# Performance work log

Hardware: AMD Instinct MI355X
Metric: run time of the kernel (lower is better)

## Reference

```python
import jax, jax.numpy as jnp
import numpy as np

H = 12            # num_heads
GRID = 14         # sqrt(num_patches)
NP_ = GRID * GRID # num_patches = 196


def _relative_position_index():
    coords = np.stack(np.meshgrid(np.arange(GRID), np.arange(GRID), indexing='ij'))  # [2,14,14]
    flat = coords.reshape(2, -1)                                   # [2,196]
    rel = flat[:, :, None] - flat[:, None, :]                      # [2,196,196]
    rel = rel.transpose(1, 2, 0).astype(np.int32)                  # [196,196,2]
    rel[..., 0] += GRID - 1
    rel[..., 1] += GRID - 1
    rel[..., 0] *= 2 * GRID - 1
    return rel.sum(-1)                                             # [196,196] in [0,729)


def setup_inputs() -> dict:
    key = jax.random.key(0)
    k1, k2, k3, k4 = jax.random.split(key, 4)
    B, N, C = 64, NP_ + 1, 768
    return {
        'x': jax.random.normal(k1, (B, N, C), dtype=jnp.float32),
        'w_qkv': jax.random.normal(k2, (3 * C, C), dtype=jnp.float32) * 0.02,
        'w_proj': jax.random.normal(k3, (C, C), dtype=jnp.float32) * 0.02,
        'b_proj': jnp.zeros((C,), dtype=jnp.float32),
        # torch inits the table to zeros; use small randn so the bias path is exercised
        'rpb_table': jax.random.normal(k4, ((2 * GRID - 1) ** 2, H), dtype=jnp.float32) * 0.02,
        'rel_idx': jnp.asarray(_relative_position_index()),
    }


def reference(x, w_qkv, w_proj, b_proj, rpb_table, rel_idx):
    B, N, C = x.shape
    hd = C // H
    scale = hd ** -0.5
    qkv = (x @ w_qkv.T).reshape(B, N, 3, H, hd).transpose(2, 0, 3, 1, 4)  # [3,B,H,N,hd]
    q, k, v = qkv[0] * scale, qkv[1], qkv[2]
    attn = jnp.einsum('bhqd,bhkd->bhqk', q, k)                            # [B,H,N,N]
    bias = rpb_table[rel_idx.reshape(-1)].reshape(NP_, NP_, H).transpose(2, 0, 1)  # [H,196,196]
    attn = attn.at[:, :, 1:, 1:].add(bias[None])                          # skip CLS row/col
    attn = jax.nn.softmax(attn, axis=-1)
    out = jnp.einsum('bhqk,bhkd->bqhd', attn, v).reshape(B, N, C)
    return out @ w_proj.T + b_proj
```

## Files before the change

### kernel.cpp

```cpp
#include <hip/hip_runtime.h>

typedef float f32x4 __attribute__((ext_vector_type(4)));
typedef short short8 __attribute__((ext_vector_type(8)));

#define DEVI static __device__ __forceinline__

DEVI ushort f2bf(float f) {
  unsigned u = __builtin_bit_cast(unsigned, f);
  u += 0x7fffu + ((u >> 16) & 1u);
  return (ushort)(u >> 16);
}

DEVI float b2f(ushort u) {
  unsigned x = ((unsigned)u) << 16;
  return __builtin_bit_cast(float, x);
}

DEVI short8 pack8(float4 a, float4 b) {
  union { ushort u[8]; short8 v; } t;
  t.u[0] = f2bf(a.x); t.u[1] = f2bf(a.y); t.u[2] = f2bf(a.z); t.u[3] = f2bf(a.w);
  t.u[4] = f2bf(b.x); t.u[5] = f2bf(b.y); t.u[6] = f2bf(b.z); t.u[7] = f2bf(b.w);
  return t.v;
}

DEVI f32x4 MFMA16(short8 a, short8 b, f32x4 c) {
  return __builtin_amdgcn_mfma_f32_16x16x32_bf16(a, b, c, 0, 0, 0);
}

DEVI void gld16(const ushort* g, ushort* l) {
  __builtin_amdgcn_global_load_lds(
      (const __attribute__((address_space(1))) unsigned int*)g,
      (__attribute__((address_space(3))) unsigned int*)l, 16, 0, 0);
}

#define VMC0() asm volatile("s_waitcnt vmcnt(0)" ::: "memory")
#define LGK0() asm volatile("s_waitcnt lgkmcnt(0)" ::: "memory")

__global__ void prep_all(const float* __restrict__ table, const int* __restrict__ rel_idx,
                         ushort* __restrict__ bias,
                         const float* __restrict__ x, ushort* __restrict__ xbf,
                         const float* __restrict__ wq, ushort* __restrict__ wqb,
                         const float* __restrict__ wp, ushort* __restrict__ wpb) {
  const int bid = blockIdx.x, tid = threadIdx.x;
  if (bid < 2028) {
    int i = bid * 256 + tid;
    int k = i % 208;
    int t = i / 208;
    int q = t % 208;
    int h = t / 208;
    float v;
    if (k >= 197) v = -1e30f;
    else if (q == 0 || k == 0 || q >= 197) v = 0.0f;
    else v = table[rel_idx[(q - 1) * 196 + (k - 1)] * 12 + h];
    bias[i] = f2bf(v);
  } else if (bid < 6756) {
    int i = (bid - 2028) * 256 + tid;
    float4 a = ((const float4*)x)[i * 2];
    float4 b = ((const float4*)x)[i * 2 + 1];
    ((short8*)xbf)[i] = pack8(a, b);
  } else if (bid < 7620) {
    int i = (bid - 6756) * 256 + tid;
    float4 a = ((const float4*)wq)[i * 2];
    float4 b = ((const float4*)wq)[i * 2 + 1];
    ((short8*)wqb)[i] = pack8(a, b);
  } else {
    int i = (bid - 7620) * 256 + tid;
    float4 a = ((const float4*)wp)[i * 2];
    float4 b = ((const float4*)wp)[i * 2 + 1];
    ((short8*)wpb)[i] = pack8(a, b);
  }
}

template <int MODE, int NBN>
__launch_bounds__(256, 4)
__global__ void gemm128(const ushort* __restrict__ A, const ushort* __restrict__ B,
                        ushort* __restrict__ q, ushort* __restrict__ k,
                        ushort* __restrict__ v,
                        const float* __restrict__ bprj, float* __restrict__ out) {
  __shared__ __align__(16) ushort As[2][4096];
  __shared__ __align__(16) ushort Bs[2][4096];

  const int tid = threadIdx.x;
  const int lane = tid & 63, wid = tid >> 6;
  const int wm = wid >> 1, wn = wid & 1;
  const int l15 = lane & 15, l4 = lane >> 4;

  const int nwg = gridDim.x;
  const int qc = nwg >> 3, rc = nwg & 7;
  const int xcd = blockIdx.x & 7, sub = blockIdx.x >> 3;
  const int wgid = (xcd < rc ? xcd * (qc + 1) : rc * (qc + 1) + (xcd - rc) * qc) + sub;
  const int bn = wgid % NBN, bm = wgid / NBN;

  const int c0 = wid * 2, c1 = wid * 2 + 1;
  const int r0 = c0 * 16 + (lane >> 2);
  const int r1 = c1 * 16 + (lane >> 2);
  const int g = lane & 3;
  const int col0 = (g << 3) ^ ((r0 & 6) << 2);
  const int col1 = (g << 3) ^ ((r1 & 6) << 2);
  long ar0 = bm * 128 + r0; if (ar0 > 12607) ar0 = 12607;
  long ar1 = bm * 128 + r1; if (ar1 > 12607) ar1 = 12607;
  const ushort* pA0 = A + ar0 * 768 + col0;
  const ushort* pA1 = A + ar1 * 768 + col1;
  const ushort* pB0 = B + (size_t)(bn * 128 + r0) * 768 + col0;
  const ushort* pB1 = B + (size_t)(bn * 128 + r1) * 768 + col1;

  const int xk = (l4 * 8) ^ ((l15 & 6) << 2);
  int aoff[4], boff[4];
#pragma unroll
  for (int m = 0; m < 4; m++) aoff[m] = (wm * 64 + m * 16 + l15) * 32 + xk;
#pragma unroll
  for (int n = 0; n < 4; n++) boff[n] = (wn * 64 + n * 16 + l15) * 32 + xk;

  f32x4 acc[4][4];
#pragma unroll
  for (int m = 0; m < 4; m++)
#pragma unroll
    for (int n = 0; n < 4; n++) acc[m][n] = (f32x4)0.0f;

#define STAGE(BUF, KO)                          \
  gld16(pA0 + (KO), &As[BUF][c0 * 512]);        \
  gld16(pA1 + (KO), &As[BUF][c1 * 512]);        \
  gld16(pB0 + (KO), &Bs[BUF][c0 * 512]);        \
  gld16(pB1 + (KO), &Bs[BUF][c1 * 512]);

#define COMPUTE(BUF)                                                \
  {                                                                 \
    short8 af[4], bv[4];                                            \
    _Pragma("unroll") for (int m = 0; m < 4; m++)                   \
        af[m] = *(const short8*)&As[BUF][aoff[m]];                  \
    _Pragma("unroll") for (int n = 0; n < 4; n++)                   \
        bv[n] = *(const short8*)&Bs[BUF][boff[n]];                  \
    __builtin_amdgcn_s_setprio(1);                                  \
    _Pragma("unroll") for (int m = 0; m < 4; m++)                   \
        _Pragma("unroll") for (int n = 0; n < 4; n++)               \
            acc[m][n] = MFMA16(af[m], bv[n], acc[m][n]);            \
    __builtin_amdgcn_s_setprio(0);                                  \
  }

  STAGE(0, 0)
  for (int t = 0; t < 23; ++t) {
    VMC0(); LGK0();
    __builtin_amdgcn_s_barrier();
    __builtin_amdgcn_sched_barrier(0);
    STAGE((t + 1) & 1, (t + 1) * 32)
    COMPUTE(t & 1)
  }
  VMC0(); LGK0();
  __builtin_amdgcn_s_barrier();
  __builtin_amdgcn_sched_barrier(0);
  COMPUTE(1)

  if (MODE == 0) {
    const int s = bn / 6;
    ushort* dst = (s == 0) ? q : ((s == 1) ? k : v);
    const float qs = (s == 0) ? 0.125f : 1.0f;
    const int cbase = bn * 128 + wn * 64 - s * 768;
    const int hh = cbase >> 6;
#pragma unroll
    for (int m = 0; m < 4; m++) {
#pragma unroll
      for (int r = 0; r < 4; r++) {
        int gm = bm * 128 + wm * 64 + m * 16 + l4 * 4 + r;
        if (gm >= 12608) continue;
        int b = gm / 197;
        int ns = gm - b * 197;
        size_t base = (size_t)((b * 12 + hh) * 197 + ns) * 64;
#pragma unroll
        for (int n = 0; n < 4; n++)
          dst[base + n * 16 + l15] = f2bf(acc[m][n][r] * qs);
      }
    }
  } else {
    float bb[4];
#pragma unroll
    for (int n = 0; n < 4; n++) bb[n] = bprj[bn * 128 + wn * 64 + n * 16 + l15];
#pragma unroll
    for (int m = 0; m < 4; m++) {
#pragma unroll
      for (int r = 0; r < 4; r++) {
        int gm = bm * 128 + wm * 64 + m * 16 + l4 * 4 + r;
        if (gm >= 12608) continue;
#pragma unroll
        for (int n = 0; n < 4; n++)
          out[(size_t)gm * 768 + bn * 128 + wn * 64 + n * 16 + l15] = acc[m][n][r] + bb[n];
      }
    }
  }
#undef STAGE
#undef COMPUTE
}

__launch_bounds__(832)
__global__ void attn(const ushort* __restrict__ qws, const ushort* __restrict__ kws,
                     const ushort* __restrict__ vws, const ushort* __restrict__ biasws,
                     ushort* __restrict__ aout) {
  __shared__ __align__(16) ushort Ks[208 * 72];
  __shared__ __align__(16) ushort Vt[64 * 232];
  __shared__ __align__(16) ushort Ps[13 * 16 * 232];

  const int bh = blockIdx.x;
  const int b = bh / 12;
  const int h = bh - b * 12;
  const ushort* qb = qws + (size_t)bh * 197 * 64;
  const ushort* kb = kws + (size_t)bh * 197 * 64;
  const ushort* vb = vws + (size_t)bh * 197 * 64;

  const int tid = threadIdx.x;
  const int lane = tid & 63, wid = tid >> 6;
  const int l15 = lane & 15, l4 = lane >> 4;

  for (int c = tid; c < 208 * 8; c += 832) {
    int n = c >> 3, col = (c & 7) << 3;
    short8 v = (short8)0;
    if (n < 197) v = *(const short8*)(kb + n * 64 + col);
    *(short8*)&Ks[n * 72 + col] = v;
  }
  for (int c = tid; c < 224 * 8; c += 832) {
    int n = c % 224;
    int d0 = (c / 224) << 3;
    ushort tmp[8] = {0, 0, 0, 0, 0, 0, 0, 0};
    if (n < 197) {
      short8 v = *(const short8*)(vb + n * 64 + d0);
#pragma unroll
      for (int j = 0; j < 8; j++) tmp[j] = (ushort)v[j];
    }
#pragma unroll
    for (int j = 0; j < 8; j++) Vt[(d0 + j) * 232 + n] = tmp[j];
  }
  __syncthreads();

  ushort* pb = &Ps[wid * (16 * 232)];
  const ushort* biasb = biasws + (size_t)h * 208 * 208;

  {
    const int t = wid;
    const int q0 = t * 16;
    int qr = q0 + l15; if (qr > 196) qr = 196;
    short8 aq0 = *(const short8*)(qb + qr * 64 + (l4 << 3));
    short8 aq1 = *(const short8*)(qb + qr * 64 + 32 + (l4 << 3));

    f32x4 sc[13];
    __builtin_amdgcn_s_setprio(1);
#pragma unroll
    for (int ct = 0; ct < 13; ct++) {
      short8 b0 = *(const short8*)&Ks[(ct * 16 + l15) * 72 + (l4 << 3)];
      short8 b1 = *(const short8*)&Ks[(ct * 16 + l15) * 72 + 32 + (l4 << 3)];
      f32x4 s = (f32x4)0.0f;
      s = MFMA16(aq0, b0, s);
      s = MFMA16(aq1, b1, s);
      sc[ct] = s;
    }
    __builtin_amdgcn_s_setprio(0);

    float mx[4] = {-1e38f, -1e38f, -1e38f, -1e38f};
#pragma unroll
    for (int ct = 0; ct < 13; ct++) {
#pragma unroll
      for (int r = 0; r < 4; r++) {
        float bv = b2f(biasb[(q0 + l4 * 4 + r) * 208 + ct * 16 + l15]);
        float v = sc[ct][r] + bv;
        sc[ct][r] = v;
        mx[r] = fmaxf(mx[r], v);
      }
    }
#pragma unroll
    for (int r = 0; r < 4; r++) {
      mx[r] = fmaxf(mx[r], __shfl_xor(mx[r], 1));
      mx[r] = fmaxf(mx[r], __shfl_xor(mx[r], 2));
      mx[r] = fmaxf(mx[r], __shfl_xor(mx[r], 4));
      mx[r] = fmaxf(mx[r], __shfl_xor(mx[r], 8));
    }
    float sum[4] = {0.f, 0.f, 0.f, 0.f};
#pragma unroll
    for (int ct = 0; ct < 13; ct++) {
#pragma unroll
      for (int r = 0; r < 4; r++) {
        float p = __expf(sc[ct][r] - mx[r]);
        sc[ct][r] = p;
        sum[r] += p;
      }
    }
#pragma unroll
    for (int r = 0; r < 4; r++) {
      sum[r] += __shfl_xor(sum[r], 1);
      sum[r] += __shfl_xor(sum[r], 2);
      sum[r] += __shfl_xor(sum[r], 4);
      sum[r] += __shfl_xor(sum[r], 8);
    }

#pragma unroll
    for (int ct = 0; ct < 13; ct++)
#pragma unroll
      for (int r = 0; r < 4; r++)
        pb[(l4 * 4 + r) * 232 + ct * 16 + l15] = f2bf(sc[ct][r]);
#pragma unroll
    for (int r = 0; r < 4; r++)
      pb[(l4 * 4 + r) * 232 + 208 + l15] = 0;

    short8 pa[7];
#pragma unroll
    for (int kk = 0; kk < 7; kk++)
      pa[kk] = *(const short8*)&pb[l15 * 232 + kk * 32 + (l4 << 3)];
    f32x4 o[4];
    __builtin_amdgcn_s_setprio(1);
#pragma unroll
    for (int dt = 0; dt < 4; dt++) {
      f32x4 acc = (f32x4)0.0f;
#pragma unroll
      for (int kk = 0; kk < 7; kk++) {
        short8 bv = *(const short8*)&Vt[(dt * 16 + l15) * 232 + kk * 32 + (l4 << 3)];
        acc = MFMA16(pa[kk], bv, acc);
      }
      o[dt] = acc;
    }
    __builtin_amdgcn_s_setprio(0);

    float rs[4];
#pragma unroll
    for (int r = 0; r < 4; r++) rs[r] = 1.0f / sum[r];
#pragma unroll
    for (int dt = 0; dt < 4; dt++) {
#pragma unroll
      for (int r = 0; r < 4; r++) {
        int row = q0 + l4 * 4 + r;
        if (row < 197) {
          float v = o[dt][r] * rs[r];
          aout[(size_t)(b * 197 + row) * 768 + h * 64 + dt * 16 + l15] = f2bf(v);
        }
      }
    }
  }
}

extern "C" void kernel_launch(void* const* d_in, const int* in_sizes, int n_in,
                              void* d_out, int out_size, void* d_ws, size_t ws_size,
                              hipStream_t stream) {
  const float* x      = (const float*)d_in[0];
  const float* w_qkv  = (const float*)d_in[1];
  const float* w_proj = (const float*)d_in[2];
  const float* b_proj = (const float*)d_in[3];
  const float* rpb    = (const float*)d_in[4];
  const int*   relidx = (const int*)d_in[5];
  float* out = (float*)d_out;

  char* ws = (char*)d_ws;
  const size_t HB = (size_t)12608 * 768 * 2;
  ushort* xbf   = (ushort*)(ws);
  ushort* qws   = (ushort*)(ws + HB);
  ushort* kws   = (ushort*)(ws + 2 * HB);
  ushort* vws   = (ushort*)(ws + 3 * HB);
  ushort* bias  = (ushort*)(ws + 4 * HB);
  ushort* wqkvb = (ushort*)(ws + 4 * HB + 2076672);
  ushort* wprjb = (ushort*)(ws + 4 * HB + 2076672 + 3538944);
  ushort* aout  = xbf;

  hipLaunchKernelGGL(prep_all, dim3(7908), dim3(256), 0, stream,
                     rpb, relidx, bias, x, xbf, w_qkv, wqkvb, w_proj, wprjb);
  hipLaunchKernelGGL((gemm128<0, 18>), dim3(18 * 99), dim3(256), 0, stream,
                     xbf, wqkvb, qws, kws, vws, nullptr, nullptr);
  hipLaunchKernelGGL(attn, dim3(768), dim3(832), 0, stream, qws, kws, vws, bias, aout);
  hipLaunchKernelGGL((gemm128<1, 6>), dim3(6 * 99), dim3(256), 0, stream,
                     aout, wprjb, nullptr, nullptr, nullptr, b_proj, out);
}
```

Baseline: 132.5 us.

## Process two query tiles per wave in attention to reuse K/V LDS fragments

Attention kernel now uses 7 waves of 448 threads instead of 13, each wave computing 32 query rows (two 16-row MFMA tiles) so every K and V fragment read from LDS feeds two MFMAs. The output stores are interleaved into the PV loop, and bias row indices are clamped for the padded rows. GEMM launch bounds are also raised to 5 waves per SIMD occupancy. This cuts LDS traffic per MFMA but raises register pressure (26 score accumulators per wave) and lowers the thread count per block. Higher GEMM occupancy may force spills.

```diff
diff --git a/kernel.cpp b/kernel.cpp
--- a/kernel.cpp
+++ b/kernel.cpp
@@ -72,7 +72,7 @@
 }
 
 template <int MODE, int NBN>
-__launch_bounds__(256, 4)
+__launch_bounds__(256, 5)
 __global__ void gemm128(const ushort* __restrict__ A, const ushort* __restrict__ B,
                         ushort* __restrict__ q, ushort* __restrict__ k,
                         ushort* __restrict__ v,
@@ -190,13 +190,13 @@
 #undef COMPUTE
 }
 
-__launch_bounds__(832)
+__launch_bounds__(448)
 __global__ void attn(const ushort* __restrict__ qws, const ushort* __restrict__ kws,
                      const ushort* __restrict__ vws, const ushort* __restrict__ biasws,
                      ushort* __restrict__ aout) {
   __shared__ __align__(16) ushort Ks[208 * 72];
   __shared__ __align__(16) ushort Vt[64 * 232];
-  __shared__ __align__(16) ushort Ps[13 * 16 * 232];
+  __shared__ __align__(16) ushort Ps[7 * 32 * 232];
 
   const int bh = blockIdx.x;
   const int b = bh / 12;
@@ -209,13 +209,13 @@
   const int lane = tid & 63, wid = tid >> 6;
   const int l15 = lane & 15, l4 = lane >> 4;
 
-  for (int c = tid; c < 208 * 8; c += 832) {
+  for (int c = tid; c < 208 * 8; c += 448) {
     int n = c >> 3, col = (c & 7) << 3;
     short8 v = (short8)0;
     if (n < 197) v = *(const short8*)(kb + n * 64 + col);
     *(short8*)&Ks[n * 72 + col] = v;
   }
-  for (int c = tid; c < 224 * 8; c += 832) {
+  for (int c = tid; c < 224 * 8; c += 448) {
     int n = c % 224;
     int d0 = (c / 224) << 3;
     ushort tmp[8] = {0, 0, 0, 0, 0, 0, 0, 0};
@@ -229,106 +229,137 @@
   }
   __syncthreads();
 
-  ushort* pb = &Ps[wid * (16 * 232)];
+  ushort* pb = &Ps[wid * (32 * 232)];
   const ushort* biasb = biasws + (size_t)h * 208 * 208;
 
   {
-    const int t = wid;
-    const int q0 = t * 16;
-    int qr = q0 + l15; if (qr > 196) qr = 196;
-    short8 aq0 = *(const short8*)(qb + qr * 64 + (l4 << 3));
-    short8 aq1 = *(const short8*)(qb + qr * 64 + 32 + (l4 << 3));
-
-    f32x4 sc[13];
+    const int q0 = wid * 32;
+    short8 aq[2][2];
+#pragma unroll
+    for (int m = 0; m < 2; m++) {
+      int qr = q0 + m * 16 + l15; if (qr > 196) qr = 196;
+      aq[m][0] = *(const short8*)(qb + qr * 64 + (l4 << 3));
+      aq[m][1] = *(const short8*)(qb + qr * 64 + 32 + (l4 << 3));
+    }
+
+    f32x4 sc[2][13];
     __builtin_amdgcn_s_setprio(1);
 #pragma unroll
     for (int ct = 0; ct < 13; ct++) {
       short8 b0 = *(const short8*)&Ks[(ct * 16 + l15) * 72 + (l4 << 3)];
       short8 b1 = *(const short8*)&Ks[(ct * 16 + l15) * 72 + 32 + (l4 << 3)];
-      f32x4 s = (f32x4)0.0f;
-      s = MFMA16(aq0, b0, s);
-      s = MFMA16(aq1, b1, s);
-      sc[ct] = s;
+#pragma unroll
+      for (int m = 0; m < 2; m++) {
+        f32x4 s = (f32x4)0.0f;
+        s = MFMA16(aq[m][0], b0, s);
+        s = MFMA16(aq[m][1], b1, s);
+        sc[m][ct] = s;
+      }
     }
     __builtin_amdgcn_s_setprio(0);
 
-    float mx[4] = {-1e38f, -1e38f, -1e38f, -1e38f};
+    float mx[2][4];
+#pragma unroll
+    for (int m = 0; m < 2; m++)
+#pragma unroll
+      for (int r = 0; r < 4; r++) mx[m][r] = -1e38f;
 #pragma unroll
     for (int ct = 0; ct < 13; ct++) {
 #pragma unroll
-      for (int r = 0; r < 4; r++) {
-        float bv = b2f(biasb[(q0 + l4 * 4 + r) * 208 + ct * 16 + l15]);
-        float v = sc[ct][r] + bv;
-        sc[ct][r] = v;
-        mx[r] = fmaxf(mx[r], v);
-      }
-    }
-#pragma unroll
-    for (int r = 0; r < 4; r++) {
-      mx[r] = fmaxf(mx[r], __shfl_xor(mx[r], 1));
-      mx[r] = fmaxf(mx[r], __shfl_xor(mx[r], 2));
-      mx[r] = fmaxf(mx[r], __shfl_xor(mx[r], 4));
-      mx[r] = fmaxf(mx[r], __shfl_xor(mx[r], 8));
-    }
-    float sum[4] = {0.f, 0.f, 0.f, 0.f};
+      for (int m = 0; m < 2; m++) {
+#pragma unroll
+        for (int r = 0; r < 4; r++) {
+          int brow = q0 + m * 16 + l4 * 4 + r; if (brow > 207) brow = 207;
+          float bv = b2f(biasb[brow * 208 + ct * 16 + l15]);
+          float v = sc[m][ct][r] + bv;
+          sc[m][ct][r] = v;
+          mx[m][r] = fmaxf(mx[m][r], v);
+        }
+      }
+    }
+#pragma unroll
+    for (int m = 0; m < 2; m++)
+#pragma unroll
+      for (int r = 0; r < 4; r++) {
+        mx[m][r] = fmaxf(mx[m][r], __shfl_xor(mx[m][r], 1));
+        mx[m][r] = fmaxf(mx[m][r], __shfl_xor(mx[m][r], 2));
+        mx[m][r] = fmaxf(mx[m][r], __shfl_xor(mx[m][r], 4));
+        mx[m][r] = fmaxf(mx[m][r], __shfl_xor(mx[m][r], 8));
+      }
+    float sum[2][4] = {{0.f, 0.f, 0.f, 0.f}, {0.f, 0.f, 0.f, 0.f}};
 #pragma unroll
     for (int ct = 0; ct < 13; ct++) {
 #pragma unroll
-      for (int r = 0; r < 4; r++) {
-        float p = __expf(sc[ct][r] - mx[r]);
-        sc[ct][r] = p;
-        sum[r] += p;
-      }
-    }
-#pragma unroll
-    for (int r = 0; r < 4; r++) {
-      sum[r] += __shfl_xor(sum[r], 1);
-      sum[r] += __shfl_xor(sum[r], 2);
-      sum[r] += __shfl_xor(sum[r], 4);
-      sum[r] += __shfl_xor(sum[r], 8);
-    }
+      for (int m = 0; m < 2; m++) {
+#pragma unroll
+        for (int r = 0; r < 4; r++) {
+          float p = __expf(sc[m][ct][r] - mx[m][r]);
+          sc[m][ct][r] = p;
+          sum[m][r] += p;
+        }
+      }
+    }
+#pragma unroll
+    for (int m = 0; m < 2; m++)
+#pragma unroll
+      for (int r = 0; r < 4; r++) {
+        sum[m][r] += __shfl_xor(sum[m][r], 1);
+        sum[m][r] += __shfl_xor(sum[m][r], 2);
+        sum[m][r] += __shfl_xor(sum[m][r], 4);
+        sum[m][r] += __shfl_xor(sum[m][r], 8);
+      }
 
 #pragma unroll
     for (int ct = 0; ct < 13; ct++)
 #pragma unroll
+      for (int m = 0; m < 2; m++)
+#pragma unroll
+        for (int r = 0; r < 4; r++)
+          pb[(m * 16 + l4 * 4 + r) * 232 + ct * 16 + l15] = f2bf(sc[m][ct][r]);
+#pragma unroll
+    for (int m = 0; m < 2; m++)
+#pragma unroll
       for (int r = 0; r < 4; r++)
-        pb[(l4 * 4 + r) * 232 + ct * 16 + l15] = f2bf(sc[ct][r]);
-#pragma unroll
-    for (int r = 0; r < 4; r++)
-      pb[(l4 * 4 + r) * 232 + 208 + l15] = 0;
-
-    short8 pa[7];
-#pragma unroll
-    for (int kk = 0; kk < 7; kk++)
-      pa[kk] = *(const short8*)&pb[l15 * 232 + kk * 32 + (l4 << 3)];
-    f32x4 o[4];
+        pb[(m * 16 + l4 * 4 + r) * 232 + 208 + l15] = 0;
+
+    short8 pa[2][7];
+#pragma unroll
+    for (int m = 0; m < 2; m++)
+#pragma unroll
+      for (int kk = 0; kk < 7; kk++)
+        pa[m][kk] = *(const short8*)&pb[(m * 16 + l15) * 232 + kk * 32 + (l4 << 3)];
+
+    float rs[2][4];
+#pragma unroll
+    for (int m = 0; m < 2; m++)
+#pragma unroll
+      for (int r = 0; r < 4; r++) rs[m][r] = 1.0f / sum[m][r];
+
     __builtin_amdgcn_s_setprio(1);
 #pragma unroll
     for (int dt = 0; dt < 4; dt++) {
-      f32x4 acc = (f32x4)0.0f;
+      f32x4 o0 = (f32x4)0.0f, o1 = (f32x4)0.0f;
 #pragma unroll
       for (int kk = 0; kk < 7; kk++) {
         short8 bv = *(const short8*)&Vt[(dt * 16 + l15) * 232 + kk * 32 + (l4 << 3)];
-        acc = MFMA16(pa[kk], bv, acc);
-      }
-      o[dt] = acc;
+        o0 = MFMA16(pa[0][kk], bv, o0);
+        o1 = MFMA16(pa[1][kk], bv, o1);
+      }
+      __builtin_amdgcn_s_setprio(0);
+#pragma unroll
+      for (int r = 0; r < 4; r++) {
+        int row0 = q0 + l4 * 4 + r;
+        if (row0 < 197)
+          aout[(size_t)(b * 197 + row0) * 768 + h * 64 + dt * 16 + l15] =
+              f2bf(o0[r] * rs[0][r]);
+        int row1 = q0 + 16 + l4 * 4 + r;
+        if (row1 < 197)
+          aout[(size_t)(b * 197 + row1) * 768 + h * 64 + dt * 16 + l15] =
+              f2bf(o1[r] * rs[1][r]);
+      }
+      __builtin_amdgcn_s_setprio(1);
     }
     __builtin_amdgcn_s_setprio(0);
-
-    float rs[4];
-#pragma unroll
-    for (int r = 0; r < 4; r++) rs[r] = 1.0f / sum[r];
-#pragma unroll
-    for (int dt = 0; dt < 4; dt++) {
-#pragma unroll
-      for (int r = 0; r < 4; r++) {
-        int row = q0 + l4 * 4 + r;
-        if (row < 197) {
-          float v = o[dt][r] * rs[r];
-          aout[(size_t)(b * 197 + row) * 768 + h * 64 + dt * 16 + l15] = f2bf(v);
-        }
-      }
-    }
   }
 }
 
@@ -358,7 +389,7 @@
                      rpb, relidx, bias, x, xbf, w_qkv, wqkvb, w_proj, wprjb);
   hipLaunchKernelGGL((gemm128<0, 18>), dim3(18 * 99), dim3(256), 0, stream,
                      xbf, wqkvb, qws, kws, vws, nullptr, nullptr);
-  hipLaunchKernelGGL(attn, dim3(768), dim3(832), 0, stream, qws, kws, vws, bias, aout);
+  hipLaunchKernelGGL(attn, dim3(768), dim3(448), 0, stream, qws, kws, vws, bias, aout);
   hipLaunchKernelGGL((gemm128<1, 6>), dim3(6 * 99), dim3(256), 0, stream,
                      aout, wprjb, nullptr, nullptr, nullptr, b_proj, out);
 }
```

New measurement: 200.6 us. 1.51x slower.
